# Performance work log

Hardware: AMD Instinct MI355X
Metric: run time of the kernel (lower is better)

Reference implementation:

```python
import jax, jax.numpy as jnp
import numpy as np

NUM_EMBEDDINGS = 1024
EMBEDDING_DIM = 64
COMMITMENT_COST = 0.25
N_TOKENS = 131072


def setup_inputs() -> dict:
    key = jax.random.key(0)
    k1, k2 = jax.random.split(key)
    inputs = jax.random.normal(k1, (N_TOKENS, EMBEDDING_DIM), dtype=jnp.float32)
    embedding_w = jax.random.normal(k2, (NUM_EMBEDDINGS, EMBEDDING_DIM), dtype=jnp.float32)
    return {"inputs": inputs, "embedding_w": embedding_w}


def reference(inputs, embedding_w):
    distances = (jnp.sum(inputs ** 2, axis=1, keepdims=True)
                 + jnp.sum(embedding_w ** 2, axis=1)
                 - 2.0 * jnp.matmul(inputs, embedding_w.T))
    encoding_indices = jnp.argmin(distances, axis=1)            # [N]
    encodings = jax.nn.one_hot(encoding_indices, NUM_EMBEDDINGS, dtype=inputs.dtype)  # [N, K]
    quantized = jnp.take(embedding_w, encoding_indices, axis=0)  # gather == one_hot @ W

    # commitment loss (quantized is detached in the torch code)
    e_latent_loss = jnp.mean((jax.lax.stop_gradient(quantized) - inputs) ** 2)
    loss = COMMITMENT_COST * e_latent_loss

    # straight-through estimator
    quantized = inputs + jax.lax.stop_gradient(quantized - inputs)

    avg_probs = jnp.mean(encodings, axis=0)                      # [K]
    perplexity = jnp.exp(-jnp.sum(avg_probs * jnp.log(avg_probs + 1e-10)))
    return loss, quantized, perplexity, encodings
```

## Files before the change

### kernel.cpp

```cpp
#include <hip/hip_runtime.h>

#define NTOK     131072
#define KCODES   1024
#define DIM      64
#define TAU_S    8e-4f

typedef unsigned short ushort_t;
typedef unsigned int uint_t;
typedef unsigned char uchar_t;
typedef __attribute__((ext_vector_type(8))) short short8;
typedef __attribute__((ext_vector_type(4))) float f32x4;
typedef __attribute__((ext_vector_type(2))) float nf32x2;


__device__ inline ushort_t f2bf(float f) {
    uint_t u = __float_as_uint(f);
    return (ushort_t)((u + 0x7FFFu + ((u >> 16) & 1u)) >> 16);
}
__device__ inline float bf2f(ushort_t h) { return __uint_as_float(((uint_t)h) << 16); }

__device__ inline void pack8(float4 p, float4 q, short8& h, short8& l) {
    float v[8] = {p.x, p.y, p.z, p.w, q.x, q.y, q.z, q.w};
#pragma unroll
    for (int j = 0; j < 8; ++j) {
        ushort_t hb = f2bf(v[j]);
        float hf = bf2f(hb);
        ushort_t lb = f2bf(v[j] - hf);
        h[j] = (short)hb;
        l[j] = (short)lb;
    }
}

__global__ __launch_bounds__(256) void vq_prep(const float* __restrict__ W,
                                               uchar_t* __restrict__ Wst,
                                               float* __restrict__ wsq,
                                               uint_t* __restrict__ counts,
                                               uchar_t* __restrict__ flagb) {
    const int tid = threadIdx.x;
    if (blockIdx.x == 0) {
#pragma unroll
        for (int j = 0; j < 4; ++j) counts[tid * 4 + j] = 0u;
    }
    const int e = blockIdx.x * 256 + tid;
    *(ushort_t*)(flagb + 2 * (size_t)e) = 0;
    const int k = e >> 6, d = e & 63;
    const float w = W[e];
    const ushort_t hb = f2bf(w);
    const float hf = bf2f(hb);
    const ushort_t lb = f2bf(w - hf);
    const int g = k >> 5, c = k & 31, s = d >> 3, p = d & 7;
    const size_t base = (size_t)g * 8192 + (size_t)s * 512
                      + (size_t)(c ^ (s & 3)) * 16 + (size_t)p * 2;
    *(ushort_t*)(Wst + base)        = hb;
    *(ushort_t*)(Wst + base + 4096) = lb;
    float sq = w * w;
#pragma unroll
    for (int off = 32; off >= 1; off >>= 1) sq += __shfl_xor(sq, off, 64);
    if ((tid & 63) == 0) wsq[e >> 6] = sq;
}

__global__ __launch_bounds__(256) void vq_fused(
    const float* __restrict__ X, const uchar_t* __restrict__ Wst,
    const float* __restrict__ wsq_g, const float* __restrict__ W,
    float* __restrict__ out, ushort_t* __restrict__ idx_g,
    uint_t* __restrict__ counts, float* __restrict__ lossA,
    uchar_t* __restrict__ flagb)
{
    const int tid   = threadIdx.x;
    const int lane  = tid & 63;
    const int wv    = tid >> 6;
    const int col16 = lane & 15;
    const int ks    = lane >> 4;
    const int TB    = blockIdx.x * 64;
    const int WB    = TB + wv * 16;

    __shared__ __align__(16) char sbuf[2][8192];
    __shared__ float s_wsq[KCODES];
    __shared__ float s_xsq[4][16];
    __shared__ int   s_idx[64];

    float* enc = out + 2 + (size_t)NTOK * DIM + (size_t)TB * KCODES;

    for (int i = tid; i < KCODES; i += 256) s_wsq[i] = -0.5f * wsq_g[i];

    short8 xh0, xh1, xl0, xl1;
    {
        const float* xr = X + (size_t)(WB + col16) * DIM + ks * 8;
        float4 a0 = *(const float4*)(xr);
        float4 a1 = *(const float4*)(xr + 4);
        float4 a2 = *(const float4*)(xr + 32);
        float4 a3 = *(const float4*)(xr + 36);
        float xsq = a0.x*a0.x + a0.y*a0.y + a0.z*a0.z + a0.w*a0.w
                  + a1.x*a1.x + a1.y*a1.y + a1.z*a1.z + a1.w*a1.w
                  + a2.x*a2.x + a2.y*a2.y + a2.z*a2.z + a2.w*a2.w
                  + a3.x*a3.x + a3.y*a3.y + a3.z*a3.z + a3.w*a3.w;
        xsq += __shfl_xor(xsq, 16, 64);
        xsq += __shfl_xor(xsq, 32, 64);
        if (lane < 16) s_xsq[wv][lane] = xsq;
        pack8(a0, a1, xh0, xl0);
        pack8(a2, a3, xh1, xl1);
    }

    short8 p0, p1;
    {
        const short8* src = (const short8*)(Wst + (size_t)tid * 16);
        p0 = src[0]; p1 = src[256];
        short8* dst = (short8*)(&sbuf[0][tid * 16]);
        dst[0] = p0; dst[256] = p1;
    }
    __syncthreads();

    float m1[4], m2[4]; int i1[4];
#pragma unroll
    for (int r = 0; r < 4; ++r) { m1[r] = -3.4e38f; m2[r] = -3.4e38f; i1[r] = 0; }

    const int rb = ks * 512 + ((col16 ^ ks) * 16);
    const nf32x2 zz = {0.f, 0.f};

    for (int g = 0; g < 32; ++g) {
        const int cb = g * 32;
        const int b  = g & 1;
        if (g < 31) {
            const short8* src = (const short8*)(Wst + (size_t)(g + 1) * 8192 + (size_t)tid * 16);
            p0 = src[0]; p1 = src[256];
        }
        {
            float* zp = enc + g * 2048 + tid * 8;
            *(nf32x2*)(zp)     = zz;
            *(nf32x2*)(zp + 2) = zz;
            *(nf32x2*)(zp + 4) = zz;
            *(nf32x2*)(zp + 6) = zz;
        }
        const char* buf = sbuf[b];
#pragma unroll
        for (int j = 0; j < 2; ++j) {
            const int off = rb + j * 256;
            short8 bh0 = *(const short8*)(buf + off);
            short8 bh1 = *(const short8*)(buf + off + 2048);
            short8 bl0 = *(const short8*)(buf + off + 4096);
            short8 bl1 = *(const short8*)(buf + off + 6144);
            const float c0 = s_wsq[cb + j * 16 + col16];
            f32x4 acc;
            acc[0] = c0; acc[1] = c0; acc[2] = c0; acc[3] = c0;
            acc = __builtin_amdgcn_mfma_f32_16x16x32_bf16(xh0, bh0, acc, 0, 0, 0);
            acc = __builtin_amdgcn_mfma_f32_16x16x32_bf16(xh1, bh1, acc, 0, 0, 0);
            acc = __builtin_amdgcn_mfma_f32_16x16x32_bf16(xh0, bl0, acc, 0, 0, 0);
            acc = __builtin_amdgcn_mfma_f32_16x16x32_bf16(xh1, bl1, acc, 0, 0, 0);
            acc = __builtin_amdgcn_mfma_f32_16x16x32_bf16(xl0, bh0, acc, 0, 0, 0);
            acc = __builtin_amdgcn_mfma_f32_16x16x32_bf16(xl1, bh1, acc, 0, 0, 0);
            const int cc = cb + j * 16 + col16;
#pragma unroll
            for (int r = 0; r < 4; ++r) {
                float v = acc[r];
                bool gt = v > m1[r];
                m2[r] = fmaxf(fminf(v, m1[r]), m2[r]);
                i1[r] = gt ? cc : i1[r];
                m1[r] = fmaxf(v, m1[r]);
            }
        }
        if (g < 31) {
            short8* dst = (short8*)(&sbuf[b ^ 1][tid * 16]);
            dst[0] = p0; dst[256] = p1;
            __syncthreads();
        }
    }

#pragma unroll
    for (int mask = 1; mask <= 8; mask <<= 1) {
#pragma unroll
        for (int r = 0; r < 4; ++r) {
            float v1 = __shfl_xor(m1[r], mask, 64);
            int   j1 = __shfl_xor(i1[r], mask, 64);
            float v2 = __shfl_xor(m2[r], mask, 64);
            bool take = (v1 > m1[r]) || (v1 == m1[r] && j1 < i1[r]);
            m2[r] = take ? fmaxf(m1[r], v2) : fmaxf(v1, m2[r]);
            m1[r] = take ? v1 : m1[r];
            i1[r] = take ? j1 : i1[r];
        }
    }

    float lsum = 0.f;
    if (col16 == 0) {
#pragma unroll
        for (int r = 0; r < 4; ++r) {
            const int trow = ks * 4 + r;
            const int tok = WB + trow;
            s_idx[wv * 16 + trow] = i1[r];
            idx_g[tok] = (ushort_t)i1[r];
            atomicAdd(&counts[i1[r]], 1u);
            if (m1[r] - m2[r] < TAU_S) {
                flagb[tok] = 1;
            } else {
                lsum += s_xsq[wv][trow] - 2.f * m1[r];
            }
        }
    }
    lsum += __shfl_xor(lsum, 16, 64);
    lsum += __shfl_xor(lsum, 32, 64);
    if (lane == 0) lossA[blockIdx.x * 4 + wv] = lsum;
    __syncthreads();

    if (tid < 64)
        enc[(size_t)tid * KCODES + s_idx[tid]] = 1.f;

    for (int i = tid; i < 64 * DIM; i += 256) {
        const int r = i >> 6, c = i & 63;
        out[1 + (size_t)(TB + r) * DIM + c] = W[(size_t)s_idx[r] * DIM + c];
    }
}

__global__ __launch_bounds__(256) void vq_refine(
    const float* __restrict__ X, const float* __restrict__ W,
    float* __restrict__ out, uint_t* __restrict__ counts,
    double* __restrict__ lossB, const uchar_t* __restrict__ flagb,
    const ushort_t* __restrict__ idx_g)
{
    const int tid = threadIdx.x;
    const int lane = tid & 63;
    const int wv = tid >> 6;
    __shared__ int s_list[512];
    __shared__ int s_n;
    __shared__ float sx[DIM];
    __shared__ double sbest[4];
    __shared__ int sbi[4];

    if (wv == 0) {
        const int base = blockIdx.x * 512;
        int run = 0;
        for (int c = 0; c < 8; ++c) {
            const int t = base + c * 64 + lane;
            const bool f = flagb[t] != 0;
            unsigned long long m = __ballot(f);
            const int pos = run + __popcll(m & ((1ull << lane) - 1ull));
            if (f) s_list[pos] = t;
            run += __popcll(m);
        }
        if (lane == 0) s_n = run;
    }
    __syncthreads();
    const int n = s_n;

    double lcorr = 0.0;
    for (int e = 0; e < n; ++e) {
        const int t   = s_list[e];
        const int old = idx_g[t];
        __syncthreads();
        if (tid < DIM) sx[tid] = X[(size_t)t * DIM + tid];
        __syncthreads();
        double best = 1e300; int bi = KCODES;
        for (int k = 0; k < 4; ++k) {
            const int c = tid * 4 + k;
            const float* wr = W + (size_t)c * DIM;
            double d = 0.0;
            for (int dd = 0; dd < DIM; ++dd) {
                double diff = (double)sx[dd] - (double)wr[dd];
                d += diff * diff;
            }
            if (d < best) { best = d; bi = c; }
        }
#pragma unroll
        for (int mask = 1; mask <= 32; mask <<= 1) {
            double db = __shfl_xor(best, mask, 64);
            int    ib = __shfl_xor(bi, mask, 64);
            if (db < best || (db == best && ib < bi)) { best = db; bi = ib; }
        }
        if (lane == 0) { sbest[wv] = best; sbi[wv] = bi; }
        __syncthreads();
        if (tid == 0) {
            for (int w = 1; w < 4; ++w)
                if (sbest[w] < best || (sbest[w] == best && sbi[w] < bi)) { best = sbest[w]; bi = sbi[w]; }
            lcorr += best;
            if (bi != old) {
                atomicSub(&counts[old], 1u);
                atomicAdd(&counts[bi], 1u);
                float* encp = out + 2 + (size_t)NTOK * DIM + (size_t)t * KCODES;
                encp[old] = 0.f; encp[bi] = 1.f;
                float* q = out + 1 + (size_t)t * DIM;
                for (int dd = 0; dd < DIM; ++dd) q[dd] = W[(size_t)bi * DIM + dd];
            }
        }
    }
    if (tid == 0) lossB[blockIdx.x] = lcorr;
}

__global__ __launch_bounds__(256) void vq_finalize(
    const uint_t* __restrict__ counts, const float* __restrict__ lossA,
    const double* __restrict__ lossB, float* __restrict__ out)
{
    int tid = threadIdx.x;
    double ls = 0.0;
    for (int i = tid; i < 8192; i += 256) ls += (double)lossA[i];
    ls += lossB[tid];
    float h = 0.f;
    for (int i = tid; i < KCODES; i += 256) {
        float p = (float)counts[i] * (1.0f / (float)NTOK);
        h += p * logf(p + 1e-10f);
    }
    __shared__ double dred[256];
    dred[tid] = ls;
    __syncthreads();
#pragma unroll
    for (int s = 128; s >= 1; s >>= 1) {
        if (tid < s) dred[tid] += dred[tid + s];
        __syncthreads();
    }
    __shared__ float red[4];
#pragma unroll
    for (int off = 32; off >= 1; off >>= 1) h += __shfl_down(h, off, 64);
    if ((tid & 63) == 0) red[tid >> 6] = h;
    __syncthreads();
    if (tid == 0) {
        float ht = red[0] + red[1] + red[2] + red[3];
        out[(size_t)NTOK * DIM + 1] = expf(-ht);
        out[0] = 0.25f * (float)(dred[0] / ((double)NTOK * DIM));
    }
}

extern "C" void kernel_launch(void* const* d_in, const int* in_sizes, int n_in,
                              void* d_out, int out_size, void* d_ws, size_t ws_size,
                              hipStream_t stream) {
    const float* X = (const float*)d_in[0];
    const float* W = (const float*)d_in[1];
    float* out = (float*)d_out;
    uint_t*   counts = (uint_t*)d_ws;
    float*    lossA  = (float*)((char*)d_ws + 4096);
    double*   lossB  = (double*)((char*)d_ws + 36864);
    float*    wsq    = (float*)((char*)d_ws + 38912);
    uchar_t*  Wst    = (uchar_t*)((char*)d_ws + 43008);
    uchar_t*  flagb  = (uchar_t*)((char*)d_ws + 305152);
    ushort_t* idx_g  = (ushort_t*)((char*)d_ws + 436224);

    vq_prep<<<256, 256, 0, stream>>>(W, Wst, wsq, counts, flagb);
    vq_fused<<<NTOK / 64, 256, 0, stream>>>(X, Wst, wsq, W, out, idx_g,
                                            counts, lossA, flagb);
    vq_refine<<<256, 256, 0, stream>>>(X, W, out, counts, lossB, flagb, idx_g);
    vq_finalize<<<1, 256, 0, stream>>>(counts, lossA, lossB, out);
}
```

Before: 238.3 us.

## Compact ambiguous tokens into atomic list and refine one token per wavefront

Tokens whose top two scores are within the tie margin are now appended to a global list through an atomic counter, replacing the per-token flag byte array that the refine kernel had to scan. The refine kernel assigns one token per wavefront, with each lane checking 16 codes in double precision and no block-level barriers. It no longer needs a block to handle 512 tokens with two syncthreads per token. The fused kernel also reads the codebook norms straight from global memory instead of staging them in shared memory. The list is capped, and tokens beyond the cap keep their approximate result without refinement, which could change results if many ties occur.

```diff
diff --git a/kernel.cpp b/kernel.cpp
--- a/kernel.cpp
+++ b/kernel.cpp
@@ -4,6 +4,7 @@
 #define KCODES   1024
 #define DIM      64
 #define TAU_S    8e-4f
+#define FLAG_CAP 16384
 
 typedef unsigned short ushort_t;
 typedef unsigned int uint_t;
@@ -35,14 +36,14 @@
                                                uchar_t* __restrict__ Wst,
                                                float* __restrict__ wsq,
                                                uint_t* __restrict__ counts,
-                                               uchar_t* __restrict__ flagb) {
+                                               uint_t* __restrict__ flag_cnt) {
     const int tid = threadIdx.x;
     if (blockIdx.x == 0) {
 #pragma unroll
         for (int j = 0; j < 4; ++j) counts[tid * 4 + j] = 0u;
+        if (tid == 0) *flag_cnt = 0u;
     }
     const int e = blockIdx.x * 256 + tid;
-    *(ushort_t*)(flagb + 2 * (size_t)e) = 0;
     const int k = e >> 6, d = e & 63;
     const float w = W[e];
     const ushort_t hb = f2bf(w);
@@ -64,7 +65,7 @@
     const float* __restrict__ wsq_g, const float* __restrict__ W,
     float* __restrict__ out, ushort_t* __restrict__ idx_g,
     uint_t* __restrict__ counts, float* __restrict__ lossA,
-    uchar_t* __restrict__ flagb)
+    uint_t* __restrict__ flag_cnt, int* __restrict__ flags)
 {
     const int tid   = threadIdx.x;
     const int lane  = tid & 63;
@@ -75,13 +76,10 @@
     const int WB    = TB + wv * 16;
 
     __shared__ __align__(16) char sbuf[2][8192];
-    __shared__ float s_wsq[KCODES];
     __shared__ float s_xsq[4][16];
     __shared__ int   s_idx[64];
 
     float* enc = out + 2 + (size_t)NTOK * DIM + (size_t)TB * KCODES;
-
-    for (int i = tid; i < KCODES; i += 256) s_wsq[i] = -0.5f * wsq_g[i];
 
     short8 xh0, xh1, xl0, xl1;
     {
@@ -120,6 +118,8 @@
     for (int g = 0; g < 32; ++g) {
         const int cb = g * 32;
         const int b  = g & 1;
+        const float c0a = -0.5f * wsq_g[cb + col16];
+        const float c0b = -0.5f * wsq_g[cb + 16 + col16];
         if (g < 31) {
             const short8* src = (const short8*)(Wst + (size_t)(g + 1) * 8192 + (size_t)tid * 16);
             p0 = src[0]; p1 = src[256];
@@ -139,7 +139,7 @@
             short8 bh1 = *(const short8*)(buf + off + 2048);
             short8 bl0 = *(const short8*)(buf + off + 4096);
             short8 bl1 = *(const short8*)(buf + off + 6144);
-            const float c0 = s_wsq[cb + j * 16 + col16];
+            const float c0 = j ? c0b : c0a;
             f32x4 acc;
             acc[0] = c0; acc[1] = c0; acc[2] = c0; acc[3] = c0;
             acc = __builtin_amdgcn_mfma_f32_16x16x32_bf16(xh0, bh0, acc, 0, 0, 0);
@@ -189,7 +189,9 @@
             idx_g[tok] = (ushort_t)i1[r];
             atomicAdd(&counts[i1[r]], 1u);
             if (m1[r] - m2[r] < TAU_S) {
-                flagb[tok] = 1;
+                uint_t pos = atomicAdd(flag_cnt, 1u);
+                if (pos < FLAG_CAP) flags[pos] = tok;
+                else lsum += s_xsq[wv][trow] - 2.f * m1[r];
             } else {
                 lsum += s_xsq[wv][trow] - 2.f * m1[r];
             }
@@ -212,51 +214,40 @@
 __global__ __launch_bounds__(256) void vq_refine(
     const float* __restrict__ X, const float* __restrict__ W,
     float* __restrict__ out, uint_t* __restrict__ counts,
-    double* __restrict__ lossB, const uchar_t* __restrict__ flagb,
-    const ushort_t* __restrict__ idx_g)
+    double* __restrict__ lossB, const uint_t* __restrict__ flag_cnt,
+    const int* __restrict__ flags, const ushort_t* __restrict__ idx_g)
 {
-    const int tid = threadIdx.x;
+    const int tid  = threadIdx.x;
     const int lane = tid & 63;
-    const int wv = tid >> 6;
-    __shared__ int s_list[512];
-    __shared__ int s_n;
-    __shared__ float sx[DIM];
-    __shared__ double sbest[4];
-    __shared__ int sbi[4];
-
-    if (wv == 0) {
-        const int base = blockIdx.x * 512;
-        int run = 0;
-        for (int c = 0; c < 8; ++c) {
-            const int t = base + c * 64 + lane;
-            const bool f = flagb[t] != 0;
-            unsigned long long m = __ballot(f);
-            const int pos = run + __popcll(m & ((1ull << lane) - 1ull));
-            if (f) s_list[pos] = t;
-            run += __popcll(m);
-        }
-        if (lane == 0) s_n = run;
-    }
-    __syncthreads();
-    const int n = s_n;
+    const int wid  = blockIdx.x * 4 + (tid >> 6);
+    uint_t n = *flag_cnt; if (n > FLAG_CAP) n = FLAG_CAP;
 
     double lcorr = 0.0;
-    for (int e = 0; e < n; ++e) {
-        const int t   = s_list[e];
+    for (uint_t e = wid; e < n; e += 1024) {
+        const int t   = flags[e];
         const int old = idx_g[t];
-        __syncthreads();
-        if (tid < DIM) sx[tid] = X[(size_t)t * DIM + tid];
-        __syncthreads();
+
+        float xf[DIM];
+        {
+            const float4* xr4 = (const float4*)(X + (size_t)t * DIM);
+#pragma unroll
+            for (int i = 0; i < 16; ++i) {
+                float4 v = xr4[i];
+                xf[4*i+0] = v.x; xf[4*i+1] = v.y; xf[4*i+2] = v.z; xf[4*i+3] = v.w;
+            }
+        }
+
         double best = 1e300; int bi = KCODES;
-        for (int k = 0; k < 4; ++k) {
-            const int c = tid * 4 + k;
+        for (int k = 0; k < 16; ++k) {
+            const int c = (k << 6) + lane;
             const float* wr = W + (size_t)c * DIM;
-            double d = 0.0;
-            for (int dd = 0; dd < DIM; ++dd) {
-                double diff = (double)sx[dd] - (double)wr[dd];
-                d += diff * diff;
-            }
-            if (d < best) { best = d; bi = c; }
+            double dsum = 0.0;
+#pragma unroll
+            for (int d = 0; d < DIM; ++d) {
+                double diff = (double)xf[d] - (double)wr[d];
+                dsum += diff * diff;
+            }
+            if (dsum < best) { best = dsum; bi = c; }
         }
 #pragma unroll
         for (int mask = 1; mask <= 32; mask <<= 1) {
@@ -264,23 +255,19 @@
             int    ib = __shfl_xor(bi, mask, 64);
             if (db < best || (db == best && ib < bi)) { best = db; bi = ib; }
         }
-        if (lane == 0) { sbest[wv] = best; sbi[wv] = bi; }
-        __syncthreads();
-        if (tid == 0) {
-            for (int w = 1; w < 4; ++w)
-                if (sbest[w] < best || (sbest[w] == best && sbi[w] < bi)) { best = sbest[w]; bi = sbi[w]; }
+        out[1 + (size_t)t * DIM + lane] = W[(size_t)bi * DIM + lane];
+        if (lane == 0) {
             lcorr += best;
             if (bi != old) {
                 atomicSub(&counts[old], 1u);
                 atomicAdd(&counts[bi], 1u);
                 float* encp = out + 2 + (size_t)NTOK * DIM + (size_t)t * KCODES;
-                encp[old] = 0.f; encp[bi] = 1.f;
-                float* q = out + 1 + (size_t)t * DIM;
-                for (int dd = 0; dd < DIM; ++dd) q[dd] = W[(size_t)bi * DIM + dd];
-            }
-        }
-    }
-    if (tid == 0) lossB[blockIdx.x] = lcorr;
+                encp[old] = 0.f;
+                encp[bi]  = 1.f;
+            }
+        }
+    }
+    if (lane == 0) lossB[wid] = lcorr;
 }
 
 __global__ __launch_bounds__(256) void vq_finalize(
@@ -290,7 +277,7 @@
     int tid = threadIdx.x;
     double ls = 0.0;
     for (int i = tid; i < 8192; i += 256) ls += (double)lossA[i];
-    ls += lossB[tid];
+    for (int i = tid; i < 1024; i += 256) ls += lossB[i];
     float h = 0.f;
     for (int i = tid; i < KCODES; i += 256) {
         float p = (float)counts[i] * (1.0f / (float)NTOK);
@@ -322,17 +309,19 @@
     const float* X = (const float*)d_in[0];
     const float* W = (const float*)d_in[1];
     float* out = (float*)d_out;
-    uint_t*   counts = (uint_t*)d_ws;
-    float*    lossA  = (float*)((char*)d_ws + 4096);
-    double*   lossB  = (double*)((char*)d_ws + 36864);
-    float*    wsq    = (float*)((char*)d_ws + 38912);
-    uchar_t*  Wst    = (uchar_t*)((char*)d_ws + 43008);
-    uchar_t*  flagb  = (uchar_t*)((char*)d_ws + 305152);
-    ushort_t* idx_g  = (ushort_t*)((char*)d_ws + 436224);
-
-    vq_prep<<<256, 256, 0, stream>>>(W, Wst, wsq, counts, flagb);
+    uint_t*   counts   = (uint_t*)d_ws;
+    uint_t*   flag_cnt = (uint_t*)((char*)d_ws + 4096);
+    float*    lossA    = (float*)((char*)d_ws + 4112);
+    double*   lossB    = (double*)((char*)d_ws + 36880);
+    float*    wsq      = (float*)((char*)d_ws + 45072);
+    uchar_t*  Wst      = (uchar_t*)((char*)d_ws + 49408);
+    int*      flags    = (int*)((char*)d_ws + 311552);
+    ushort_t* idx_g    = (ushort_t*)((char*)d_ws + 377088);
+
+    vq_prep<<<256, 256, 0, stream>>>(W, Wst, wsq, counts, flag_cnt);
     vq_fused<<<NTOK / 64, 256, 0, stream>>>(X, Wst, wsq, W, out, idx_g,
-                                            counts, lossA, flagb);
-    vq_refine<<<256, 256, 0, stream>>>(X, W, out, counts, lossB, flagb, idx_g);
+                                            counts, lossA, flag_cnt, flags);
+    vq_refine<<<256, 256, 0, stream>>>(X, W, out, counts, lossB,
+                                       flag_cnt, flags, idx_g);
     vq_finalize<<<1, 256, 0, stream>>>(counts, lossA, lossB, out);
 }
```

Measured after the change: 216.1 us. -9.3%, faster.
